# Performance work log

Measured on AMD Instinct MI355X. Metric: run time of the kernel, lower is better.

Reference implementation:

```python
import jax, jax.numpy as jnp
import numpy as np

B_, L_, DIN, DM, DS, DR, K = 2, 1024, 1024, 2048, 16, 128, 4


def setup_inputs() -> dict:
    key = jax.random.key(0)
    ks = jax.random.split(key, 10)
    s = lambda k, shape, sc=0.02: (jax.random.normal(k, shape, jnp.float32) * sc)
    A_init = jnp.tile(jnp.arange(1, DS + 1, dtype=jnp.float32)[None, :], (DM, 1))  # (DM, DS)
    return {
        'x_in': jax.random.normal(ks[0], (B_, L_, DIN), jnp.float32),
        'W_in': s(ks[1], (DIN, DM)),
        'W_res': s(ks[2], (DIN, DM)),
        'W_out': s(ks[3], (DM, DIN)),
        'conv_w': s(ks[4], (DM, K), 0.1),   # depthwise conv weight (torch shape (DM,1,K) squeezed)
        'conv_b': jnp.zeros((DM,), jnp.float32),
        'A_log': jnp.log(A_init),
        'D': jnp.ones((DM,), jnp.float32),
        'W_B': s(ks[5], (DM, DS)),
        'W_C': s(ks[6], (DM, DS)),
        'W_dt': s(ks[7], (DM, DR)),
        'dt_w': s(ks[8], (DR, DM)),
        'dt_b': jnp.zeros((DM,), jnp.float32),
    }


def reference(x_in, W_in, W_res, W_out, conv_w, conv_b, A_log, D, W_B, W_C, W_dt, dt_w, dt_b):
    Bb, L, _ = x_in.shape
    x = x_in @ W_in                     # (B, L, DM)
    res = x_in @ W_res                  # (B, L, DM)
    # Causal depthwise conv1d: pad left k-1, truncate to L (matches Conv1d(padding=k-1)[:, :, :L])
    xp = jnp.pad(x, ((0, 0), (K - 1, 0), (0, 0)))
    xc = conv_b
    for i in range(K):
        xc = xc + xp[:, i:i + L, :] * conv_w[:, i]
    xc = jax.nn.silu(xc)                # (B, L, DM)
    # Selective SSM (fused_ssm)
    A = -jnp.exp(A_log)                 # (DM, DS)
    Bp = xc @ W_B                       # (B, L, DS)
    Cp = xc @ W_C                       # (B, L, DS)
    delta = jax.nn.softplus((xc @ W_dt) @ dt_w + dt_b)  # (B, L, DM)
    dA = jnp.exp(delta[..., None] * A)                       # (B, L, DM, DS)
    dBu = delta[..., None] * Bp[:, :, None, :] * xc[..., None]  # (B, L, DM, DS)

    def step(h, inp):
        dA_t, dBu_t, C_t = inp
        h = dA_t * h + dBu_t                         # (B, DM, DS)
        y = jnp.einsum('bdn,bn->bd', h, C_t)         # (B, DM)
        return h, y

    h0 = jnp.zeros((Bb, DM, DS), jnp.float32)
    _, ys = jax.lax.scan(step, h0, (dA.transpose(1, 0, 2, 3), dBu.transpose(1, 0, 2, 3), Cp.transpose(1, 0, 2)))
    y = ys.transpose(1, 0, 2) + D * xc  # (B, L, DM)
    y = y * jax.nn.silu(res)
    return y @ W_out                    # (B, L, DIN)
```

## Files before the change

kernel.cpp:

```cpp
#include <hip/hip_runtime.h>
#include <hip/hip_bf16.h>

constexpr int B_  = 2;
constexpr int L_  = 1024;
constexpr int DIN = 1024;
constexpr int DM  = 2048;
constexpr int DS  = 16;
constexpr int DR  = 128;
constexpr int KC  = 4;
constexpr int M_  = B_ * L_;
constexpr int NP2 = 256;
constexpr int KSLICES = 8;
constexpr int KSL = DM / KSLICES;

constexpr int NC = 32;
constexpr int CL = L_ / NC;
constexpr int S_ = B_ * DM * DS;

typedef __bf16 bf16x8 __attribute__((ext_vector_type(8)));
typedef float  f32x4  __attribute__((ext_vector_type(4)));

__device__ __forceinline__ void gload_lds16(const void* g, void* l) {
    __builtin_amdgcn_global_load_lds(
        (const __attribute__((address_space(1))) void*)g,
        (__attribute__((address_space(3))) void*)l, 16, 0, 0);
}

__device__ __forceinline__ void transpose_block(const float* __restrict__ in,
                                                __bf16* __restrict__ out,
                                                int R, int C, int bx, int by, int t) {
    __shared__ float tile[32][33];
    int tx = t & 31, ty = t >> 5;
    #pragma unroll
    for (int j = 0; j < 32; j += 8)
        tile[ty + j][tx] = in[(size_t)(by * 32 + ty + j) * C + (bx * 32 + tx)];
    __syncthreads();
    #pragma unroll
    for (int j = 0; j < 32; j += 8)
        out[(size_t)(bx * 32 + ty + j) * R + (by * 32 + tx)] = (__bf16)tile[tx][ty + j];
}

__global__ void prep_all(const float* __restrict__ x_in, const float* __restrict__ W_in,
                         const float* __restrict__ W_res, const float* __restrict__ W_out,
                         const float* __restrict__ dt_w,
                         const float* __restrict__ W_B, const float* __restrict__ W_C,
                         const float* __restrict__ W_dt, const float* __restrict__ conv_w,
                         __bf16* __restrict__ xinB, __bf16* __restrict__ WinT,
                         __bf16* __restrict__ WresT, __bf16* __restrict__ WoutT,
                         __bf16* __restrict__ dtwT, __bf16* __restrict__ projW,
                         float* __restrict__ cwT) {
    int blk = blockIdx.x, t = threadIdx.x;
    if (blk < 8192) {
        int i = blk * 256 + t;
        xinB[i] = (__bf16)x_in[i];
    } else if (blk < 10240) {
        int b = blk - 8192;
        transpose_block(W_in, WinT, DIN, DM, b % 64, b / 64, t);
    } else if (blk < 12288) {
        int b = blk - 10240;
        transpose_block(W_res, WresT, DIN, DM, b % 64, b / 64, t);
    } else if (blk < 14336) {
        int b = blk - 12288;
        transpose_block(W_out, WoutT, DM, DIN, b % 32, b / 32, t);
    } else if (blk < 14592) {
        int b = blk - 14336;
        transpose_block(dt_w, dtwT, DR, DM, b % 64, b / 64, t);
    } else if (blk < 16640) {
        int i = (blk - 14592) * 256 + t;
        int k = i % DM;
        int n = i / DM;
        float v = 0.f;
        if (n < 16)        v = W_B[(size_t)k * DS + n];
        else if (n < 32)   v = W_C[(size_t)k * DS + (n - 16)];
        else if (n < 160)  v = W_dt[(size_t)k * DR + (n - 32)];
        projW[i] = (__bf16)v;
    } else {
        int j = (blk - 16640) * 256 + t;
        int tap = j / DM, d = j % DM;
        cwT[j] = conv_w[d * KC + tap];
    }
}

__global__ void reduce_split(const float* __restrict__ Ppart, float* __restrict__ Bp,
                             float* __restrict__ Cp, __bf16* __restrict__ dtmpB) {
    int i = blockIdx.x * 256 + threadIdx.x;
    int row = i / 160, c = i % 160;
    float v = 0.f;
    #pragma unroll
    for (int ks = 0; ks < KSLICES; ks++)
        v += Ppart[(size_t)ks * M_ * NP2 + (size_t)row * NP2 + c];
    if (c < 16)       Bp[(size_t)row * DS + c] = v;
    else if (c < 32)  Cp[(size_t)row * DS + (c - 16)] = v;
    else              dtmpB[(size_t)row * DR + (c - 32)] = (__bf16)v;
}

template<int EPI>
__global__ void gemm_tile128(const __bf16* __restrict__ A, const __bf16* __restrict__ BT,
                             float* __restrict__ Cf, __bf16* __restrict__ Cb,
                             const float* __restrict__ bias, int M, int N, int K,
                             int lda, int ldb) {
    __shared__ __bf16 sA[128 * 32];
    __shared__ __bf16 sB[128 * 32];
    int t = threadIdx.x;
    int lane = t & 63, w = t >> 6;
    int wm = w >> 1, wn = w & 1;
    int m0 = blockIdx.y * 128, n0 = blockIdx.x * 128;
    int kbase = blockIdx.z * K;
    int q = lane >> 4, rr = lane & 15;

    f32x4 acc[4][4] = {};

    int srow = t >> 2;
    int slot = t & 3;

    for (int kt = 0; kt < K; kt += 32) {
        __syncthreads();
        #pragma unroll
        for (int rnd = 0; rnd < 2; rnd++) {
            int row = srow + rnd * 64;
            int gkb = slot ^ ((row >> 1) & 3);
            const __bf16* ga = A  + (size_t)(m0 + row) * lda + kbase + kt + gkb * 8;
            const __bf16* gb = BT + (size_t)(n0 + row) * ldb + kbase + kt + gkb * 8;
            __bf16* la = sA + rnd * 2048 + w * 512;
            __bf16* lb = sB + rnd * 2048 + w * 512;
            gload_lds16(ga, la);
            gload_lds16(gb, lb);
        }
        __syncthreads();

        bf16x8 af[4], bfr[4];
        #pragma unroll
        for (int i = 0; i < 4; i++) {
            int rowA = wm * 64 + i * 16 + rr;
            af[i] = *(const bf16x8*)(sA + rowA * 32 + ((q ^ ((rowA >> 1) & 3)) * 8));
            int rowB = wn * 64 + i * 16 + rr;
            bfr[i] = *(const bf16x8*)(sB + rowB * 32 + ((q ^ ((rowB >> 1) & 3)) * 8));
        }
        #pragma unroll
        for (int i = 0; i < 4; i++)
            #pragma unroll
            for (int j = 0; j < 4; j++)
                acc[i][j] = __builtin_amdgcn_mfma_f32_16x16x32_bf16(af[i], bfr[j], acc[i][j], 0, 0, 0);
    }

    float* Cz = Cf + (size_t)blockIdx.z * M * N;
    #pragma unroll
    for (int i = 0; i < 4; i++) {
        #pragma unroll
        for (int j = 0; j < 4; j++) {
            int col = n0 + wn * 64 + j * 16 + rr;
            #pragma unroll
            for (int jj = 0; jj < 4; jj++) {
                int row = m0 + wm * 64 + i * 16 + q * 4 + jj;
                float v = acc[i][j][jj];
                if (EPI == 0) {
                    Cz[(size_t)row * N + col] = v;
                } else if (EPI == 1) {
                    float z = v + bias[col];
                    Cb[(size_t)row * N + col] = (__bf16)((z > 20.f) ? z : log1pf(__expf(z)));
                } else {
                    if (col < DM) ((__bf16*)Cf)[(size_t)row * DM + col] = (__bf16)v;
                    else          Cb[(size_t)row * DM + (col - DM)] = (__bf16)v;
                }
            }
        }
    }
}

__global__ void gemm_out64(const __bf16* __restrict__ A, const __bf16* __restrict__ BT,
                           float* __restrict__ C, int M, int N, int K, int lda, int ldb) {
    __shared__ __bf16 sA[128 * 32];
    __shared__ __bf16 sB[64 * 32];
    int t = threadIdx.x;
    int lane = t & 63, w = t >> 6;
    int m0 = blockIdx.y * 128, n0 = blockIdx.x * 64;
    int q = lane >> 4, rr = lane & 15;

    f32x4 acc[2][4] = {};
    int srow = t >> 2;
    int slot = t & 3;

    for (int kt = 0; kt < K; kt += 32) {
        __syncthreads();
        #pragma unroll
        for (int rnd = 0; rnd < 2; rnd++) {
            int row = srow + rnd * 64;
            int gkb = slot ^ ((row >> 1) & 3);
            const __bf16* ga = A + (size_t)(m0 + row) * lda + kt + gkb * 8;
            __bf16* la = sA + rnd * 2048 + w * 512;
            gload_lds16(ga, la);
        }
        {
            int row = srow;
            int gkb = slot ^ ((row >> 1) & 3);
            const __bf16* gb = BT + (size_t)(n0 + row) * ldb + kt + gkb * 8;
            __bf16* lb = sB + w * 512;
            gload_lds16(gb, lb);
        }
        __syncthreads();

        bf16x8 af[2], bfr[4];
        #pragma unroll
        for (int i = 0; i < 2; i++) {
            int rowA = w * 32 + i * 16 + rr;
            af[i] = *(const bf16x8*)(sA + rowA * 32 + ((q ^ ((rowA >> 1) & 3)) * 8));
        }
        #pragma unroll
        for (int j = 0; j < 4; j++) {
            int rowB = j * 16 + rr;
            bfr[j] = *(const bf16x8*)(sB + rowB * 32 + ((q ^ ((rowB >> 1) & 3)) * 8));
        }
        #pragma unroll
        for (int i = 0; i < 2; i++)
            #pragma unroll
            for (int j = 0; j < 4; j++)
                acc[i][j] = __builtin_amdgcn_mfma_f32_16x16x32_bf16(af[i], bfr[j], acc[i][j], 0, 0, 0);
    }

    #pragma unroll
    for (int i = 0; i < 2; i++) {
        #pragma unroll
        for (int j = 0; j < 4; j++) {
            int col = n0 + j * 16 + rr;
            #pragma unroll
            for (int jj = 0; jj < 4; jj++) {
                int row = m0 + w * 32 + i * 16 + q * 4 + jj;
                C[(size_t)row * N + col] = acc[i][j][jj];
            }
        }
    }
}

__global__ void conv_silu(const __bf16* __restrict__ x, const float* __restrict__ cwT,
                          const float* __restrict__ bias, __bf16* __restrict__ xcB) {
    int row = blockIdx.x;
    int d   = threadIdx.x * 8;
    int l   = row % L_;
    size_t base = (size_t)row * DM + d;

    float acc[8];
    {
        const f32x4* b4 = (const f32x4*)(bias + d);
        f32x4 b0 = b4[0], b1 = b4[1];
        #pragma unroll
        for (int q = 0; q < 4; q++) { acc[q] = b0[q]; acc[4 + q] = b1[q]; }
    }
    #pragma unroll
    for (int i = 0; i < KC; i++) {
        int li = l - (KC - 1) + i;
        if (li >= 0) {
            bf16x8 xv = *(const bf16x8*)(x + base + (size_t)(i - (KC - 1)) * DM);
            const f32x4* w4 = (const f32x4*)(cwT + (size_t)i * DM + d);
            f32x4 w0 = w4[0], w1 = w4[1];
            #pragma unroll
            for (int q = 0; q < 4; q++) {
                acc[q]     = fmaf((float)xv[q],     w0[q], acc[q]);
                acc[4 + q] = fmaf((float)xv[4 + q], w1[q], acc[4 + q]);
            }
        }
    }
    bf16x8 out;
    #pragma unroll
    for (int q = 0; q < 8; q++) {
        float v = acc[q] / (1.f + __expf(-acc[q]));
        out[q] = (__bf16)v;
    }
    *(bf16x8*)(xcB + base) = out;
}

__global__ void scan_phase1(const __bf16* __restrict__ delta, const __bf16* __restrict__ xc,
                            const float* __restrict__ Bp, const float* __restrict__ A_log,
                            __bf16* __restrict__ aprodB, __bf16* __restrict__ cendB) {
    int blk = blockIdx.x;
    int c   = blk % NC;
    int rem = blk / NC;
    int dmt = rem % (DM / 256);
    int b   = rem / (DM / 256);
    int t   = threadIdx.x;
    int dm  = dmt * 256 + t;
    int l0  = c * CL;

    __shared__ float sB[CL * DS];
    sB[t]       = Bp[((size_t)b * L_ + l0) * DS + t];
    sB[t + 256] = Bp[((size_t)b * L_ + l0) * DS + t + 256];
    __syncthreads();

    float Aval[DS];
    {
        const f32x4* Ap = (const f32x4*)(A_log + (size_t)dm * DS);
        #pragma unroll
        for (int r4 = 0; r4 < 4; r4++) {
            f32x4 a = Ap[r4];
            #pragma unroll
            for (int q = 0; q < 4; q++) Aval[r4 * 4 + q] = -__expf(a[q]);
        }
    }

    float h[DS], ap[DS];
    #pragma unroll
    for (int i = 0; i < DS; i++) { h[i] = 0.f; ap[i] = 1.f; }

    size_t base = ((size_t)b * L_ + l0) * DM + dm;
    #pragma unroll 4
    for (int j = 0; j < CL; j++) {
        float dl  = (float)delta[base + (size_t)j * DM];
        float xv  = (float)xc[base + (size_t)j * DM];
        float cmn = dl * xv;
        const f32x4* sB4 = (const f32x4*)(sB + j * DS);
        #pragma unroll
        for (int r4 = 0; r4 < 4; r4++) {
            f32x4 bv = sB4[r4];
            #pragma unroll
            for (int q = 0; q < 4; q++) {
                int i = r4 * 4 + q;
                float dA = __expf(dl * Aval[i]);
                ap[i] *= dA;
                h[i] = fmaf(dA, h[i], cmn * bv[q]);
            }
        }
    }

    size_t s = ((size_t)(b * DM + dm)) * DS;
    #pragma unroll
    for (int r8 = 0; r8 < 2; r8++) {
        bf16x8 va, vh;
        #pragma unroll
        for (int q = 0; q < 8; q++) { va[q] = (__bf16)ap[r8 * 8 + q]; vh[q] = (__bf16)h[r8 * 8 + q]; }
        ((bf16x8*)(aprodB + (size_t)c * S_ + s))[r8] = va;
        ((bf16x8*)(cendB  + (size_t)c * S_ + s))[r8] = vh;
    }
}

__global__ void scan_phase2(const __bf16* __restrict__ aprodB, const __bf16* __restrict__ cendB,
                            __bf16* __restrict__ hinitB) {
    int u8 = (blockIdx.x * 256 + threadIdx.x) * 8;
    float h[8];
    #pragma unroll
    for (int q = 0; q < 8; q++) h[q] = 0.f;
    #pragma unroll
    for (int c = 0; c < NC; c++) {
        bf16x8 a = *(const bf16x8*)(aprodB + (size_t)c * S_ + u8);
        bf16x8 ce = *(const bf16x8*)(cendB + (size_t)c * S_ + u8);
        bf16x8 ho;
        #pragma unroll
        for (int q = 0; q < 8; q++) {
            ho[q] = (__bf16)h[q];
            h[q] = fmaf((float)a[q], h[q], (float)ce[q]);
        }
        *(bf16x8*)(hinitB + (size_t)c * S_ + u8) = ho;
    }
}

__global__ void scan_phase3(const __bf16* __restrict__ delta, const __bf16* __restrict__ xc,
                            const float* __restrict__ Bp, const float* __restrict__ Cp,
                            const __bf16* __restrict__ res, const float* __restrict__ A_log,
                            const float* __restrict__ Dw, const __bf16* __restrict__ hinitB,
                            __bf16* __restrict__ ybar) {
    int blk = blockIdx.x;
    int c   = blk % NC;
    int rem = blk / NC;
    int dmt = rem % (DM / 256);
    int b   = rem / (DM / 256);
    int t   = threadIdx.x;
    int dm  = dmt * 256 + t;
    int l0  = c * CL;

    __shared__ float sB[CL * DS];
    __shared__ float sC[CL * DS];
    sB[t]       = Bp[((size_t)b * L_ + l0) * DS + t];
    sB[t + 256] = Bp[((size_t)b * L_ + l0) * DS + t + 256];
    sC[t]       = Cp[((size_t)b * L_ + l0) * DS + t];
    sC[t + 256] = Cp[((size_t)b * L_ + l0) * DS + t + 256];
    __syncthreads();

    float Aval[DS];
    {
        const f32x4* Ap = (const f32x4*)(A_log + (size_t)dm * DS);
        #pragma unroll
        for (int r4 = 0; r4 < 4; r4++) {
            f32x4 a = Ap[r4];
            #pragma unroll
            for (int q = 0; q < 4; q++) Aval[r4 * 4 + q] = -__expf(a[q]);
        }
    }
    float Dval = Dw[dm];

    float h[DS];
    {
        size_t s = ((size_t)(b * DM + dm)) * DS;
        #pragma unroll
        for (int r8 = 0; r8 < 2; r8++) {
            bf16x8 v = ((const bf16x8*)(hinitB + (size_t)c * S_ + s))[r8];
            #pragma unroll
            for (int q = 0; q < 8; q++) h[r8 * 8 + q] = (float)v[q];
        }
    }

    size_t base = ((size_t)b * L_ + l0) * DM + dm;
    #pragma unroll 4
    for (int j = 0; j < CL; j++) {
        float dl  = (float)delta[base + (size_t)j * DM];
        float xv  = (float)xc[base + (size_t)j * DM];
        float rv  = (float)res[base + (size_t)j * DM];
        float cmn = dl * xv;
        float y = 0.f;
        const f32x4* sB4 = (const f32x4*)(sB + j * DS);
        const f32x4* sC4 = (const f32x4*)(sC + j * DS);
        #pragma unroll
        for (int r4 = 0; r4 < 4; r4++) {
            f32x4 bv = sB4[r4];
            f32x4 cv = sC4[r4];
            #pragma unroll
            for (int q = 0; q < 4; q++) {
                int i = r4 * 4 + q;
                float dA = __expf(dl * Aval[i]);
                h[i] = fmaf(dA, h[i], cmn * bv[q]);
                y = fmaf(h[i], cv[q], y);
            }
        }
        float g = rv / (1.f + __expf(-rv));
        ybar[base + (size_t)j * DM] = (__bf16)((y + Dval * xv) * g);
    }
}

extern "C" void kernel_launch(void* const* d_in, const int* in_sizes, int n_in,
                              void* d_out, int out_size, void* d_ws, size_t ws_size,
                              hipStream_t stream) {
    const float* x_in   = (const float*)d_in[0];
    const float* W_in   = (const float*)d_in[1];
    const float* W_res  = (const float*)d_in[2];
    const float* W_out  = (const float*)d_in[3];
    const float* conv_w = (const float*)d_in[4];
    const float* conv_b = (const float*)d_in[5];
    const float* A_log  = (const float*)d_in[6];
    const float* Dw     = (const float*)d_in[7];
    const float* W_B    = (const float*)d_in[8];
    const float* W_C    = (const float*)d_in[9];
    const float* W_dt   = (const float*)d_in[10];
    const float* dt_w   = (const float*)d_in[11];
    const float* dt_b   = (const float*)d_in[12];

    float* ws_f = (float*)d_ws;
    float* Ppart = ws_f;
    float* Bp    = Ppart + (size_t)KSLICES * M_ * NP2;
    float* Cp    = Bp    + (size_t)M_ * DS;
    float* cwT   = Cp    + (size_t)M_ * DS;
    __bf16* bf_base = (__bf16*)(cwT + (size_t)KC * DM);
    __bf16* ybar   = bf_base;
    __bf16* xinB   = ybar   + (size_t)M_ * DM;
    __bf16* WinT   = xinB   + (size_t)M_ * DIN;
    __bf16* WresT  = WinT   + (size_t)DM * DIN;
    __bf16* WoutT  = WresT  + (size_t)DM * DIN;
    __bf16* xB     = WoutT  + (size_t)DIN * DM;
    __bf16* xcB    = xB     + (size_t)M_ * DM;
    __bf16* projW  = xcB    + (size_t)M_ * DM;
    __bf16* dtwT   = projW  + (size_t)NP2 * DM;
    __bf16* dtmpB  = dtwT   + (size_t)DM * DR;
    __bf16* deltaB = dtmpB  + (size_t)M_ * DR;
    __bf16* resB   = deltaB + (size_t)M_ * DM;
    __bf16* aprodB = resB   + (size_t)M_ * DM;
    __bf16* cendB  = aprodB + (size_t)NC * S_;
    __bf16* hinitB = cendB  + (size_t)NC * S_;

    prep_all<<<16672, 256, 0, stream>>>(x_in, W_in, W_res, W_out, dt_w, W_B, W_C, W_dt,
                                        conv_w, xinB, WinT, WresT, WoutT, dtwT, projW, cwT);

    gemm_tile128<2><<<dim3((2 * DM) / 128, M_ / 128, 1), 256, 0, stream>>>(
        xinB, WinT, (float*)xB, resB, nullptr, M_, 2 * DM, DIN, DIN, DIN);

    conv_silu<<<M_, 256, 0, stream>>>(xB, cwT, conv_b, xcB);

    gemm_tile128<0><<<dim3(NP2 / 128, M_ / 128, KSLICES), 256, 0, stream>>>(
        xcB, projW, Ppart, nullptr, nullptr, M_, NP2, KSL, DM, DM);
    reduce_split<<<(M_ * 160) / 256, 256, 0, stream>>>(Ppart, Bp, Cp, dtmpB);

    gemm_tile128<1><<<dim3(DM / 128, M_ / 128, 1), 256, 0, stream>>>(
        dtmpB, dtwT, nullptr, deltaB, dt_b, M_, DM, DR, DR, DR);

    int nblk = B_ * (DM / 256) * NC;
    scan_phase1<<<nblk, 256, 0, stream>>>(deltaB, xcB, Bp, A_log, aprodB, cendB);
    scan_phase2<<<S_ / (256 * 8), 256, 0, stream>>>(aprodB, cendB, hinitB);
    scan_phase3<<<nblk, 256, 0, stream>>>(deltaB, xcB, Bp, Cp, resB, A_log, Dw, hinitB, ybar);

    gemm_out64<<<dim3(DIN / 64, M_ / 128), 256, 0, stream>>>(
        ybar, WoutT, (float*)d_out, M_, DIN, DM, DM, DM);
}
```

Baseline: 267.1 us.

## Fuse split-K reduction via atomics, read fp32 P in delta GEMM, cooperative fused scan

The split-K projection GEMM now accumulates its partial sums straight into a single zeroed fp32 buffer with atomicAdd, which removes the separate reduce_split kernel and the eight-slice partial buffer. A new delta GEMM reads the dt-rank activations directly from that fp32 buffer and converts them to bf16 on the fly. The three scan phases are merged into one cooperative kernel with grid-wide syncs, which removes two launches and lets each block keep its loaded B/C tiles in shared memory. The costs are atomic contention, nondeterministic summation order, extra zeroing work in prep, and a cooperative launch that requires all 512 blocks to be co-resident.

Result: slower. 508.5 us (+90.4%).

```diff
diff --git a/kernel.cpp b/kernel.cpp
--- a/kernel.cpp
+++ b/kernel.cpp
@@ -1,5 +1,8 @@
 #include <hip/hip_runtime.h>
 #include <hip/hip_bf16.h>
+#include <hip/hip_cooperative_groups.h>
+
+namespace cg = cooperative_groups;
 
 constexpr int B_  = 2;
 constexpr int L_  = 1024;
@@ -48,7 +51,7 @@
                          __bf16* __restrict__ xinB, __bf16* __restrict__ WinT,
                          __bf16* __restrict__ WresT, __bf16* __restrict__ WoutT,
                          __bf16* __restrict__ dtwT, __bf16* __restrict__ projW,
-                         float* __restrict__ cwT) {
+                         float* __restrict__ cwT, float* __restrict__ P) {
     int blk = blockIdx.x, t = threadIdx.x;
     if (blk < 8192) {
         int i = blk * 256 + t;
@@ -74,24 +77,14 @@
         else if (n < 32)   v = W_C[(size_t)k * DS + (n - 16)];
         else if (n < 160)  v = W_dt[(size_t)k * DR + (n - 32)];
         projW[i] = (__bf16)v;
-    } else {
+    } else if (blk < 16672) {
         int j = (blk - 16640) * 256 + t;
         int tap = j / DM, d = j % DM;
         cwT[j] = conv_w[d * KC + tap];
-    }
-}
-
-__global__ void reduce_split(const float* __restrict__ Ppart, float* __restrict__ Bp,
-                             float* __restrict__ Cp, __bf16* __restrict__ dtmpB) {
-    int i = blockIdx.x * 256 + threadIdx.x;
-    int row = i / 160, c = i % 160;
-    float v = 0.f;
-    #pragma unroll
-    for (int ks = 0; ks < KSLICES; ks++)
-        v += Ppart[(size_t)ks * M_ * NP2 + (size_t)row * NP2 + c];
-    if (c < 16)       Bp[(size_t)row * DS + c] = v;
-    else if (c < 32)  Cp[(size_t)row * DS + (c - 16)] = v;
-    else              dtmpB[(size_t)row * DR + (c - 32)] = (__bf16)v;
+    } else {
+        int i = (blk - 16672) * 256 + t;
+        ((f32x4*)P)[i] = f32x4{0.f, 0.f, 0.f, 0.f};
+    }
 }
 
 template<int EPI>
@@ -158,10 +151,74 @@
                 } else if (EPI == 1) {
                     float z = v + bias[col];
                     Cb[(size_t)row * N + col] = (__bf16)((z > 20.f) ? z : log1pf(__expf(z)));
-                } else {
+                } else if (EPI == 2) {
                     if (col < DM) ((__bf16*)Cf)[(size_t)row * DM + col] = (__bf16)v;
                     else          Cb[(size_t)row * DM + (col - DM)] = (__bf16)v;
+                } else {
+                    if (col < 160) atomicAdd(&Cf[(size_t)row * N + col], v);
                 }
+            }
+        }
+    }
+}
+
+__global__ void gemm_delta(const float* __restrict__ P, const __bf16* __restrict__ BT,
+                           const float* __restrict__ bias, __bf16* __restrict__ Cb,
+                           int M, int N) {
+    __shared__ __bf16 sB[128 * 32];
+    int t = threadIdx.x;
+    int lane = t & 63, w = t >> 6;
+    int wm = w >> 1, wn = w & 1;
+    int m0 = blockIdx.y * 128, n0 = blockIdx.x * 128;
+    int q = lane >> 4, rr = lane & 15;
+
+    f32x4 acc[4][4] = {};
+    int srow = t >> 2;
+    int slot = t & 3;
+
+    for (int kt = 0; kt < DR; kt += 32) {
+        __syncthreads();
+        #pragma unroll
+        for (int rnd = 0; rnd < 2; rnd++) {
+            int row = srow + rnd * 64;
+            int gkb = slot ^ ((row >> 1) & 3);
+            const __bf16* gb = BT + (size_t)(n0 + row) * DR + kt + gkb * 8;
+            __bf16* lb = sB + rnd * 2048 + w * 512;
+            gload_lds16(gb, lb);
+        }
+        __syncthreads();
+
+        bf16x8 af[4], bfr[4];
+        #pragma unroll
+        for (int i = 0; i < 4; i++) {
+            int rowA = m0 + wm * 64 + i * 16 + rr;
+            const f32x4* ap = (const f32x4*)(P + (size_t)rowA * NP2 + 32 + kt + q * 8);
+            f32x4 a0 = ap[0], a1 = ap[1];
+            bf16x8 av;
+            #pragma unroll
+            for (int c = 0; c < 4; c++) { av[c] = (__bf16)a0[c]; av[4 + c] = (__bf16)a1[c]; }
+            af[i] = av;
+            int rowB = wn * 64 + i * 16 + rr;
+            bfr[i] = *(const bf16x8*)(sB + rowB * 32 + ((q ^ ((rowB >> 1) & 3)) * 8));
+        }
+        #pragma unroll
+        for (int i = 0; i < 4; i++)
+            #pragma unroll
+            for (int j = 0; j < 4; j++)
+                acc[i][j] = __builtin_amdgcn_mfma_f32_16x16x32_bf16(af[i], bfr[j], acc[i][j], 0, 0, 0);
+    }
+
+    #pragma unroll
+    for (int i = 0; i < 4; i++) {
+        #pragma unroll
+        for (int j = 0; j < 4; j++) {
+            int col = n0 + wn * 64 + j * 16 + rr;
+            float bz = bias[col];
+            #pragma unroll
+            for (int jj = 0; jj < 4; jj++) {
+                int row = m0 + wm * 64 + i * 16 + q * 4 + jj;
+                float z = acc[i][j][jj] + bz;
+                Cb[(size_t)row * N + col] = (__bf16)((z > 20.f) ? z : log1pf(__expf(z)));
             }
         }
     }
@@ -268,9 +325,13 @@
     *(bf16x8*)(xcB + base) = out;
 }
 
-__global__ void scan_phase1(const __bf16* __restrict__ delta, const __bf16* __restrict__ xc,
-                            const float* __restrict__ Bp, const float* __restrict__ A_log,
-                            __bf16* __restrict__ aprodB, __bf16* __restrict__ cendB) {
+__global__ void scan_fused(const __bf16* __restrict__ delta, const __bf16* __restrict__ xc,
+                           const float* __restrict__ P, const float* __restrict__ A_log,
+                           const float* __restrict__ Dw, const __bf16* __restrict__ res,
+                           __bf16* __restrict__ aprodB, __bf16* __restrict__ cendB,
+                           __bf16* __restrict__ hinitB, __bf16* __restrict__ ybar) {
+    cg::grid_group grid = cg::this_grid();
+
     int blk = blockIdx.x;
     int c   = blk % NC;
     int rem = blk / NC;
@@ -281,8 +342,16 @@
     int l0  = c * CL;
 
     __shared__ float sB[CL * DS];
-    sB[t]       = Bp[((size_t)b * L_ + l0) * DS + t];
-    sB[t + 256] = Bp[((size_t)b * L_ + l0) * DS + t + 256];
+    __shared__ float sC[CL * DS];
+    {
+        size_t prow0 = ((size_t)b * L_ + l0 + (t >> 4)) * NP2;
+        size_t prow1 = ((size_t)b * L_ + l0 + 16 + (t >> 4)) * NP2;
+        int cidx = t & 15;
+        sB[t]       = P[prow0 + cidx];
+        sB[t + 256] = P[prow1 + cidx];
+        sC[t]       = P[prow0 + 16 + cidx];
+        sC[t + 256] = P[prow1 + 16 + cidx];
+    }
     __syncthreads();
 
     float Aval[DS];
@@ -295,131 +364,102 @@
             for (int q = 0; q < 4; q++) Aval[r4 * 4 + q] = -__expf(a[q]);
         }
     }
-
-    float h[DS], ap[DS];
-    #pragma unroll
-    for (int i = 0; i < DS; i++) { h[i] = 0.f; ap[i] = 1.f; }
+    float Dval = Dw[dm];
 
     size_t base = ((size_t)b * L_ + l0) * DM + dm;
-    #pragma unroll 4
-    for (int j = 0; j < CL; j++) {
-        float dl  = (float)delta[base + (size_t)j * DM];
-        float xv  = (float)xc[base + (size_t)j * DM];
-        float cmn = dl * xv;
-        const f32x4* sB4 = (const f32x4*)(sB + j * DS);
-        #pragma unroll
-        for (int r4 = 0; r4 < 4; r4++) {
-            f32x4 bv = sB4[r4];
-            #pragma unroll
-            for (int q = 0; q < 4; q++) {
-                int i = r4 * 4 + q;
-                float dA = __expf(dl * Aval[i]);
-                ap[i] *= dA;
-                h[i] = fmaf(dA, h[i], cmn * bv[q]);
-            }
-        }
-    }
-
     size_t s = ((size_t)(b * DM + dm)) * DS;
-    #pragma unroll
-    for (int r8 = 0; r8 < 2; r8++) {
-        bf16x8 va, vh;
-        #pragma unroll
-        for (int q = 0; q < 8; q++) { va[q] = (__bf16)ap[r8 * 8 + q]; vh[q] = (__bf16)h[r8 * 8 + q]; }
-        ((bf16x8*)(aprodB + (size_t)c * S_ + s))[r8] = va;
-        ((bf16x8*)(cendB  + (size_t)c * S_ + s))[r8] = vh;
-    }
-}
-
-__global__ void scan_phase2(const __bf16* __restrict__ aprodB, const __bf16* __restrict__ cendB,
-                            __bf16* __restrict__ hinitB) {
-    int u8 = (blockIdx.x * 256 + threadIdx.x) * 8;
-    float h[8];
-    #pragma unroll
-    for (int q = 0; q < 8; q++) h[q] = 0.f;
-    #pragma unroll
-    for (int c = 0; c < NC; c++) {
-        bf16x8 a = *(const bf16x8*)(aprodB + (size_t)c * S_ + u8);
-        bf16x8 ce = *(const bf16x8*)(cendB + (size_t)c * S_ + u8);
-        bf16x8 ho;
-        #pragma unroll
-        for (int q = 0; q < 8; q++) {
-            ho[q] = (__bf16)h[q];
-            h[q] = fmaf((float)a[q], h[q], (float)ce[q]);
-        }
-        *(bf16x8*)(hinitB + (size_t)c * S_ + u8) = ho;
-    }
-}
-
-__global__ void scan_phase3(const __bf16* __restrict__ delta, const __bf16* __restrict__ xc,
-                            const float* __restrict__ Bp, const float* __restrict__ Cp,
-                            const __bf16* __restrict__ res, const float* __restrict__ A_log,
-                            const float* __restrict__ Dw, const __bf16* __restrict__ hinitB,
-                            __bf16* __restrict__ ybar) {
-    int blk = blockIdx.x;
-    int c   = blk % NC;
-    int rem = blk / NC;
-    int dmt = rem % (DM / 256);
-    int b   = rem / (DM / 256);
-    int t   = threadIdx.x;
-    int dm  = dmt * 256 + t;
-    int l0  = c * CL;
-
-    __shared__ float sB[CL * DS];
-    __shared__ float sC[CL * DS];
-    sB[t]       = Bp[((size_t)b * L_ + l0) * DS + t];
-    sB[t + 256] = Bp[((size_t)b * L_ + l0) * DS + t + 256];
-    sC[t]       = Cp[((size_t)b * L_ + l0) * DS + t];
-    sC[t + 256] = Cp[((size_t)b * L_ + l0) * DS + t + 256];
-    __syncthreads();
-
-    float Aval[DS];
+
     {
-        const f32x4* Ap = (const f32x4*)(A_log + (size_t)dm * DS);
-        #pragma unroll
-        for (int r4 = 0; r4 < 4; r4++) {
-            f32x4 a = Ap[r4];
-            #pragma unroll
-            for (int q = 0; q < 4; q++) Aval[r4 * 4 + q] = -__expf(a[q]);
-        }
-    }
-    float Dval = Dw[dm];
-
-    float h[DS];
+        float h[DS], ap[DS];
+        #pragma unroll
+        for (int i = 0; i < DS; i++) { h[i] = 0.f; ap[i] = 1.f; }
+
+        #pragma unroll 4
+        for (int j = 0; j < CL; j++) {
+            float dl  = (float)delta[base + (size_t)j * DM];
+            float xv  = (float)xc[base + (size_t)j * DM];
+            float cmn = dl * xv;
+            const f32x4* sB4 = (const f32x4*)(sB + j * DS);
+            #pragma unroll
+            for (int r4 = 0; r4 < 4; r4++) {
+                f32x4 bv = sB4[r4];
+                #pragma unroll
+                for (int q = 0; q < 4; q++) {
+                    int i = r4 * 4 + q;
+                    float dA = __expf(dl * Aval[i]);
+                    ap[i] *= dA;
+                    h[i] = fmaf(dA, h[i], cmn * bv[q]);
+                }
+            }
+        }
+        #pragma unroll
+        for (int r8 = 0; r8 < 2; r8++) {
+            bf16x8 va, vh;
+            #pragma unroll
+            for (int q = 0; q < 8; q++) { va[q] = (__bf16)ap[r8 * 8 + q]; vh[q] = (__bf16)h[r8 * 8 + q]; }
+            ((bf16x8*)(aprodB + (size_t)c * S_ + s))[r8] = va;
+            ((bf16x8*)(cendB  + (size_t)c * S_ + s))[r8] = vh;
+        }
+    }
+
+    __threadfence();
+    grid.sync();
+
+    if (blk < S_ / (256 * 8)) {
+        int u8 = (blk * 256 + t) * 8;
+        float h[8];
+        #pragma unroll
+        for (int q = 0; q < 8; q++) h[q] = 0.f;
+        #pragma unroll
+        for (int cc = 0; cc < NC; cc++) {
+            bf16x8 a  = *(const bf16x8*)(aprodB + (size_t)cc * S_ + u8);
+            bf16x8 ce = *(const bf16x8*)(cendB  + (size_t)cc * S_ + u8);
+            bf16x8 ho;
+            #pragma unroll
+            for (int q = 0; q < 8; q++) {
+                ho[q] = (__bf16)h[q];
+                h[q] = fmaf((float)a[q], h[q], (float)ce[q]);
+            }
+            *(bf16x8*)(hinitB + (size_t)cc * S_ + u8) = ho;
+        }
+    }
+
+    __threadfence();
+    grid.sync();
+
     {
-        size_t s = ((size_t)(b * DM + dm)) * DS;
+        float h[DS];
         #pragma unroll
         for (int r8 = 0; r8 < 2; r8++) {
             bf16x8 v = ((const bf16x8*)(hinitB + (size_t)c * S_ + s))[r8];
             #pragma unroll
             for (int q = 0; q < 8; q++) h[r8 * 8 + q] = (float)v[q];
         }
-    }
-
-    size_t base = ((size_t)b * L_ + l0) * DM + dm;
-    #pragma unroll 4
-    for (int j = 0; j < CL; j++) {
-        float dl  = (float)delta[base + (size_t)j * DM];
-        float xv  = (float)xc[base + (size_t)j * DM];
-        float rv  = (float)res[base + (size_t)j * DM];
-        float cmn = dl * xv;
-        float y = 0.f;
-        const f32x4* sB4 = (const f32x4*)(sB + j * DS);
-        const f32x4* sC4 = (const f32x4*)(sC + j * DS);
-        #pragma unroll
-        for (int r4 = 0; r4 < 4; r4++) {
-            f32x4 bv = sB4[r4];
-            f32x4 cv = sC4[r4];
-            #pragma unroll
-            for (int q = 0; q < 4; q++) {
-                int i = r4 * 4 + q;
-                float dA = __expf(dl * Aval[i]);
-                h[i] = fmaf(dA, h[i], cmn * bv[q]);
-                y = fmaf(h[i], cv[q], y);
-            }
-        }
-        float g = rv / (1.f + __expf(-rv));
-        ybar[base + (size_t)j * DM] = (__bf16)((y + Dval * xv) * g);
+
+        #pragma unroll 4
+        for (int j = 0; j < CL; j++) {
+            float dl  = (float)delta[base + (size_t)j * DM];
+            float xv  = (float)xc[base + (size_t)j * DM];
+            float rv  = (float)res[base + (size_t)j * DM];
+            float cmn = dl * xv;
+            float y = 0.f;
+            const f32x4* sB4 = (const f32x4*)(sB + j * DS);
+            const f32x4* sC4 = (const f32x4*)(sC + j * DS);
+            #pragma unroll
+            for (int r4 = 0; r4 < 4; r4++) {
+                f32x4 bv = sB4[r4];
+                f32x4 cv = sC4[r4];
+                #pragma unroll
+                for (int q = 0; q < 4; q++) {
+                    int i = r4 * 4 + q;
+                    float dA = __expf(dl * Aval[i]);
+                    h[i] = fmaf(dA, h[i], cmn * bv[q]);
+                    y = fmaf(h[i], cv[q], y);
+                }
+            }
+            float g = rv / (1.f + __expf(-rv));
+            ybar[base + (size_t)j * DM] = (__bf16)((y + Dval * xv) * g);
+        }
     }
 }
 
@@ -441,10 +481,8 @@
     const float* dt_b   = (const float*)d_in[12];
 
     float* ws_f = (float*)d_ws;
-    float* Ppart = ws_f;
-    float* Bp    = Ppart + (size_t)KSLICES * M_ * NP2;
-    float* Cp    = Bp    + (size_t)M_ * DS;
-    float* cwT   = Cp    + (size_t)M_ * DS;
+    float* P     = ws_f;
+    float* cwT   = P + (size_t)M_ * NP2;
     __bf16* bf_base = (__bf16*)(cwT + (size_t)KC * DM);
     __bf16* ybar   = bf_base;
     __bf16* xinB   = ybar   + (size_t)M_ * DM;
@@ -455,32 +493,34 @@
     __bf16* xcB    = xB     + (size_t)M_ * DM;
     __bf16* projW  = xcB    + (size_t)M_ * DM;
     __bf16* dtwT   = projW  + (size_t)NP2 * DM;
-    __bf16* dtmpB  = dtwT   + (size_t)DM * DR;
-    __bf16* deltaB = dtmpB  + (size_t)M_ * DR;
+    __bf16* deltaB = dtwT   + (size_t)DM * DR;
     __bf16* resB   = deltaB + (size_t)M_ * DM;
     __bf16* aprodB = resB   + (size_t)M_ * DM;
     __bf16* cendB  = aprodB + (size_t)NC * S_;
     __bf16* hinitB = cendB  + (size_t)NC * S_;
 
-    prep_all<<<16672, 256, 0, stream>>>(x_in, W_in, W_res, W_out, dt_w, W_B, W_C, W_dt,
-                                        conv_w, xinB, WinT, WresT, WoutT, dtwT, projW, cwT);
+    prep_all<<<17184, 256, 0, stream>>>(x_in, W_in, W_res, W_out, dt_w, W_B, W_C, W_dt,
+                                        conv_w, xinB, WinT, WresT, WoutT, dtwT, projW,
+                                        cwT, P);
 
     gemm_tile128<2><<<dim3((2 * DM) / 128, M_ / 128, 1), 256, 0, stream>>>(
         xinB, WinT, (float*)xB, resB, nullptr, M_, 2 * DM, DIN, DIN, DIN);
 
     conv_silu<<<M_, 256, 0, stream>>>(xB, cwT, conv_b, xcB);
 
-    gemm_tile128<0><<<dim3(NP2 / 128, M_ / 128, KSLICES), 256, 0, stream>>>(
-        xcB, projW, Ppart, nullptr, nullptr, M_, NP2, KSL, DM, DM);
-    reduce_split<<<(M_ * 160) / 256, 256, 0, stream>>>(Ppart, Bp, Cp, dtmpB);
-
-    gemm_tile128<1><<<dim3(DM / 128, M_ / 128, 1), 256, 0, stream>>>(
-        dtmpB, dtwT, nullptr, deltaB, dt_b, M_, DM, DR, DR, DR);
-
-    int nblk = B_ * (DM / 256) * NC;
-    scan_phase1<<<nblk, 256, 0, stream>>>(deltaB, xcB, Bp, A_log, aprodB, cendB);
-    scan_phase2<<<S_ / (256 * 8), 256, 0, stream>>>(aprodB, cendB, hinitB);
-    scan_phase3<<<nblk, 256, 0, stream>>>(deltaB, xcB, Bp, Cp, resB, A_log, Dw, hinitB, ybar);
+    gemm_tile128<3><<<dim3(NP2 / 128, M_ / 128, KSLICES), 256, 0, stream>>>(
+        xcB, projW, P, nullptr, nullptr, M_, NP2, KSL, DM, DM);
+
+    gemm_delta<<<dim3(DM / 128, M_ / 128), 256, 0, stream>>>(
+        P, dtwT, dt_b, deltaB, M_, DM);
+
+    {
+        void* args[] = {(void*)&deltaB, (void*)&xcB, (void*)&P, (void*)&A_log,
+                        (void*)&Dw, (void*)&resB, (void*)&aprodB, (void*)&cendB,
+                        (void*)&hinitB, (void*)&ybar};
+        hipLaunchCooperativeKernel((void*)scan_fused, dim3(B_ * (DM / 256) * NC), dim3(256),
+                                   args, 0, stream);
+    }
 
     gemm_out64<<<dim3(DIN / 64, M_ / 128), 256, 0, stream>>>(
         ybar, WoutT, (float*)d_out, M_, DIN, DM, DM, DM);
```
